# Kernel tuning notes

Measured on AMD Instinct MI355X. Metric: run time of the kernel, lower is better.

The kernel has to match this reference:

```python
import jax, jax.numpy as jnp
import numpy as np

N, E = 100000, 1600000
IN, H, OUT, EA = 128, 128, 128, 128
NUM_LAYERS = 4
EPS = 1e-5


def setup_inputs() -> dict:
    key = jax.random.key(0)
    ks = jax.random.split(key, 12)
    s = 0.05  # small init scale for numerical sanity
    inp = {
        "x": jax.random.normal(ks[0], (N, IN), jnp.float32),
        "edge_index": jax.random.randint(ks[1], (2, E), 0, N, dtype=jnp.int32),
        "edge_attr": jax.random.normal(ks[2], (E, EA), jnp.float32),
        # MLP linears: in->H, H->H, H->H, H->OUT
        "W0": jax.random.normal(ks[3], (H, IN), jnp.float32) * s,
        "b0": jnp.zeros((H,), jnp.float32),
        "W1": jax.random.normal(ks[4], (H, H), jnp.float32) * s,
        "b1": jnp.zeros((H,), jnp.float32),
        "W2": jax.random.normal(ks[5], (H, H), jnp.float32) * s,
        "b2": jnp.zeros((H,), jnp.float32),
        "W3": jax.random.normal(ks[6], (OUT, H), jnp.float32) * s,
        "b3": jnp.zeros((OUT,), jnp.float32),
        # EdgeConv linear: concat(x_j[H], edge_attr[EA]) -> H
        "Wc": jax.random.normal(ks[7], (H, H + EA), jnp.float32) * s,
        "bc": jnp.zeros((H,), jnp.float32),
        # BatchNorm (eval mode: running stats)
        "bn_gamma": jnp.ones((H,), jnp.float32),
        "bn_beta": jnp.zeros((H,), jnp.float32),
        "bn_mean": jnp.zeros((H,), jnp.float32),
        "bn_var": jnp.ones((H,), jnp.float32),
    }
    return inp


def _edge_conv(h, src, dst, ea, deg_inv, Wc, bc):
    # message: lin(concat(x_j, edge_attr)) per edge; aggregate: mean over dst
    msg = jnp.concatenate([h[src], ea], axis=1) @ Wc.T + bc  # [E+N, H]
    agg = jax.ops.segment_sum(msg, dst, num_segments=N)      # [N, H]
    return agg * deg_inv[:, None]


def reference(x, edge_index, edge_attr, W0, b0, W1, b1, W2, b2, W3, b3,
              Wc, bc, bn_gamma, bn_beta, bn_mean, bn_var):
    loop = jnp.arange(N, dtype=edge_index.dtype)
    src = jnp.concatenate([edge_index[0], loop])  # self-loops appended
    dst = jnp.concatenate([edge_index[1], loop])
    ea = jnp.concatenate([edge_attr, jnp.zeros((N, EA), edge_attr.dtype)], axis=0)
    deg = jax.ops.segment_sum(jnp.ones((src.shape[0],), x.dtype), dst, num_segments=N)
    deg_inv = 1.0 / deg  # >= 1 thanks to self-loops

    layers = [(W0, b0), (W1, b1), (W2, b2), (W3, b3)]
    h = x
    for i, (W, b) in enumerate(layers):
        h = h @ W.T                                   # [N, H]
        h = _edge_conv(h, src, dst, ea, deg_inv, Wc, bc)  # eval-mode propagation
        h = h + b
        if i != NUM_LAYERS - 1:
            # BatchNorm1d eval: normalize by running stats
            h = (h - bn_mean) * jax.lax.rsqrt(bn_var + EPS) * bn_gamma + bn_beta
            h = jnp.tanh(h)
            # dropout p=0.0 / eval mode: no-op
    return h
```

## Files before the change

### kernel.cpp

```cpp
#include <hip/hip_runtime.h>
#include <hip/hip_bf16.h>
#include <math.h>

#define NN 100000
#define EE 1600000
#define HD 128
#define MAXDEG 64
#define EPS_BN 1e-5f

typedef __attribute__((ext_vector_type(8))) short short8;
typedef __attribute__((ext_vector_type(4))) float f32x4;

__device__ inline float bf_hi(unsigned u) { return __uint_as_float(u & 0xffff0000u); }
__device__ inline float bf_lo(unsigned u) { return __uint_as_float(u << 16); }
__device__ inline unsigned pack_bf2(float x0, float x1) {
    __hip_bfloat16 a = __float2bfloat16(x0);
    __hip_bfloat16 b = __float2bfloat16(x1);
    unsigned short ua = *reinterpret_cast<unsigned short*>(&a);
    unsigned short ub = *reinterpret_cast<unsigned short*>(&b);
    return (unsigned)ua | ((unsigned)ub << 16);
}

__global__ __launch_bounds__(256) void mega_k(const float* __restrict__ x, unsigned* __restrict__ xb,
                                              const int* __restrict__ src, const int* __restrict__ dst,
                                              int* __restrict__ cursor, int2* __restrict__ list,
                                              const float* __restrict__ W0, const float* __restrict__ W1,
                                              const float* __restrict__ W2, const float* __restrict__ W3,
                                              const float* __restrict__ Wc,
                                              __hip_bfloat16* __restrict__ Mb,
                                              __hip_bfloat16* __restrict__ Wceb) {
    int t = blockIdx.x * 256 + threadIdx.x;
    {
        size_t base = (size_t)t * 8;
        float4 a = *(const float4*)&x[base];
        float4 b = *(const float4*)&x[base + 4];
        uint4 w;
        w.x = pack_bf2(a.x, a.y); w.y = pack_bf2(a.z, a.w);
        w.z = pack_bf2(b.x, b.y); w.w = pack_bf2(b.z, b.w);
        *(uint4*)&xb[(size_t)t * 4] = w;
    }
    {
        int v = dst[t];
        int p = atomicAdd(&cursor[v], 1);
        if (p < MAXDEG) list[(size_t)v * MAXDEG + p] = make_int2(t, src[t]);
    }
    if (blockIdx.x < 320) {
        int part = blockIdx.x >> 6;
        int idx = ((blockIdx.x & 63) << 8) + threadIdx.x;
        int o = idx >> 7, k = idx & 127;
        if (part < 4) {
            const float* W = (part == 0) ? W0 : (part == 1) ? W1 : (part == 2) ? W2 : W3;
            float s = 0.f;
            for (int j = 0; j < 128; ++j) s += Wc[o * 256 + j] * W[j * 128 + k];
            Mb[part * 16384 + idx] = __float2bfloat16(s);
        } else {
            Wceb[idx] = __float2bfloat16(Wc[o * 256 + 128 + k]);
        }
    }
}

__global__ __launch_bounds__(256) void agg_ea_k(const float* __restrict__ ea,
                                                const int* __restrict__ deg, const int2* __restrict__ list,
                                                unsigned* __restrict__ A) {
    int v = blockIdx.x * 4 + (threadIdx.x >> 6);
    int lane = threadIdx.x & 63;
    int grp = lane >> 5, lr = lane & 31;
    if (v >= NN) return;
    size_t o = (size_t)v * MAXDEG;
    int d = deg[v]; if (d > MAXDEG) d = MAXDEG;
    float a0 = 0.f, a1 = 0.f, a2 = 0.f, a3 = 0.f;
    float c0 = 0.f, c1 = 0.f, c2 = 0.f, c3 = 0.f;
    int j = grp;
    for (; j + 6 < d; j += 8) {
        int e0 = list[o + j].x;
        int e1 = list[o + j + 2].x;
        int e2 = list[o + j + 4].x;
        int e3 = list[o + j + 6].x;
        float4 r0 = *(const float4*)&ea[(size_t)e0 * HD + lr * 4];
        float4 r1 = *(const float4*)&ea[(size_t)e1 * HD + lr * 4];
        float4 r2 = *(const float4*)&ea[(size_t)e2 * HD + lr * 4];
        float4 r3 = *(const float4*)&ea[(size_t)e3 * HD + lr * 4];
        a0 += r0.x + r1.x; a1 += r0.y + r1.y; a2 += r0.z + r1.z; a3 += r0.w + r1.w;
        c0 += r2.x + r3.x; c1 += r2.y + r3.y; c2 += r2.z + r3.z; c3 += r2.w + r3.w;
    }
    for (; j + 2 < d; j += 4) {
        int e0 = list[o + j].x;
        int e1 = list[o + j + 2].x;
        float4 r0 = *(const float4*)&ea[(size_t)e0 * HD + lr * 4];
        float4 r1 = *(const float4*)&ea[(size_t)e1 * HD + lr * 4];
        a0 += r0.x + r1.x; a1 += r0.y + r1.y; a2 += r0.z + r1.z; a3 += r0.w + r1.w;
    }
    for (; j < d; j += 2) {
        int e = list[o + j].x;
        float4 r = *(const float4*)&ea[(size_t)e * HD + lr * 4];
        a0 += r.x; a1 += r.y; a2 += r.z; a3 += r.w;
    }
    a0 += c0; a1 += c1; a2 += c2; a3 += c3;
    a0 += __shfl_xor(a0, 32); a1 += __shfl_xor(a1, 32);
    a2 += __shfl_xor(a2, 32); a3 += __shfl_xor(a3, 32);
    if (grp == 0) {
        uint2 w;
        w.x = pack_bf2(a0, a1); w.y = pack_bf2(a2, a3);
        *(uint2*)&A[(size_t)v * 64 + lr * 2] = w;
    }
}

__global__ __launch_bounds__(256) void gather_sum_k(const unsigned* __restrict__ tab,
                                                    const int* __restrict__ deg, const int2* __restrict__ list,
                                                    unsigned* __restrict__ S) {
    int v = blockIdx.x * 4 + (threadIdx.x >> 6);
    int lane = threadIdx.x & 63;
    int grp = lane >> 4, lr = lane & 15;
    if (v >= NN) return;
    size_t o = (size_t)v * MAXDEG;
    int d = deg[v]; if (d > MAXDEG) d = MAXDEG;
    float acc[8], acc2[8];
    {
        uint4 r = *(const uint4*)&tab[(size_t)v * 64 + lr * 4];
        bool m = (grp == 0);
        acc[0] = m ? bf_lo(r.x) : 0.f; acc[1] = m ? bf_hi(r.x) : 0.f;
        acc[2] = m ? bf_lo(r.y) : 0.f; acc[3] = m ? bf_hi(r.y) : 0.f;
        acc[4] = m ? bf_lo(r.z) : 0.f; acc[5] = m ? bf_hi(r.z) : 0.f;
        acc[6] = m ? bf_lo(r.w) : 0.f; acc[7] = m ? bf_hi(r.w) : 0.f;
    }
#pragma unroll
    for (int i = 0; i < 8; ++i) acc2[i] = 0.f;
    int j = grp;
    for (; j + 12 < d; j += 16) {
        int s0 = list[o + j].y;
        int s1 = list[o + j + 4].y;
        int s2 = list[o + j + 8].y;
        int s3 = list[o + j + 12].y;
        uint4 r0 = *(const uint4*)&tab[(size_t)s0 * 64 + lr * 4];
        uint4 r1 = *(const uint4*)&tab[(size_t)s1 * 64 + lr * 4];
        uint4 r2 = *(const uint4*)&tab[(size_t)s2 * 64 + lr * 4];
        uint4 r3 = *(const uint4*)&tab[(size_t)s3 * 64 + lr * 4];
        acc[0] += bf_lo(r0.x) + bf_lo(r1.x); acc[1] += bf_hi(r0.x) + bf_hi(r1.x);
        acc[2] += bf_lo(r0.y) + bf_lo(r1.y); acc[3] += bf_hi(r0.y) + bf_hi(r1.y);
        acc[4] += bf_lo(r0.z) + bf_lo(r1.z); acc[5] += bf_hi(r0.z) + bf_hi(r1.z);
        acc[6] += bf_lo(r0.w) + bf_lo(r1.w); acc[7] += bf_hi(r0.w) + bf_hi(r1.w);
        acc2[0] += bf_lo(r2.x) + bf_lo(r3.x); acc2[1] += bf_hi(r2.x) + bf_hi(r3.x);
        acc2[2] += bf_lo(r2.y) + bf_lo(r3.y); acc2[3] += bf_hi(r2.y) + bf_hi(r3.y);
        acc2[4] += bf_lo(r2.z) + bf_lo(r3.z); acc2[5] += bf_hi(r2.z) + bf_hi(r3.z);
        acc2[6] += bf_lo(r2.w) + bf_lo(r3.w); acc2[7] += bf_hi(r2.w) + bf_hi(r3.w);
    }
    for (; j + 4 < d; j += 8) {
        int s0 = list[o + j].y;
        int s1 = list[o + j + 4].y;
        uint4 r0 = *(const uint4*)&tab[(size_t)s0 * 64 + lr * 4];
        uint4 r1 = *(const uint4*)&tab[(size_t)s1 * 64 + lr * 4];
        acc[0] += bf_lo(r0.x) + bf_lo(r1.x); acc[1] += bf_hi(r0.x) + bf_hi(r1.x);
        acc[2] += bf_lo(r0.y) + bf_lo(r1.y); acc[3] += bf_hi(r0.y) + bf_hi(r1.y);
        acc[4] += bf_lo(r0.z) + bf_lo(r1.z); acc[5] += bf_hi(r0.z) + bf_hi(r1.z);
        acc[6] += bf_lo(r0.w) + bf_lo(r1.w); acc[7] += bf_hi(r0.w) + bf_hi(r1.w);
    }
    for (; j < d; j += 4) {
        int s = list[o + j].y;
        uint4 r = *(const uint4*)&tab[(size_t)s * 64 + lr * 4];
        acc[0] += bf_lo(r.x); acc[1] += bf_hi(r.x);
        acc[2] += bf_lo(r.y); acc[3] += bf_hi(r.y);
        acc[4] += bf_lo(r.z); acc[5] += bf_hi(r.z);
        acc[6] += bf_lo(r.w); acc[7] += bf_hi(r.w);
    }
#pragma unroll
    for (int i = 0; i < 8; ++i) {
        acc[i] += acc2[i];
        acc[i] += __shfl_xor(acc[i], 16);
        acc[i] += __shfl_xor(acc[i], 32);
    }
    if (grp == 0) {
        uint4 w;
        w.x = pack_bf2(acc[0], acc[1]); w.y = pack_bf2(acc[2], acc[3]);
        w.z = pack_bf2(acc[4], acc[5]); w.w = pack_bf2(acc[6], acc[7]);
        *(uint4*)&S[(size_t)v * 64 + lr * 4] = w;
    }
}

template <int MODE>
__global__ __launch_bounds__(256) void gemm_epi_k(const __hip_bfloat16* __restrict__ Sb,
                                                  const __hip_bfloat16* __restrict__ Bw,
                                                  uint2* __restrict__ Usw,
                                                  const int* __restrict__ deg,
                                                  const float* __restrict__ bias,
                                                  const float* __restrict__ bng, const float* __restrict__ bnb,
                                                  const float* __restrict__ bnm, const float* __restrict__ bnv,
                                                  void* __restrict__ out) {
    int wave = threadIdx.x >> 6, lane = threadIdx.x & 63;
    int r0 = blockIdx.x * 64 + wave * 16;
    int R = blockIdx.x * 4 + wave;
    int lr = lane & 15, lg = lane >> 4;

    f32x4 acc[8];
#pragma unroll
    for (int i = 0; i < 8; ++i) acc[i] = (f32x4){0.f, 0.f, 0.f, 0.f};

    int arow = r0 + lr;
    if (arow >= NN) arow = NN - 1;

#pragma unroll
    for (int kb = 0; kb < 4; ++kb) {
        int kofs = kb * 32 + lg * 8;
        short8 a = *(const short8*)(Sb + (size_t)arow * HD + kofs);
#pragma unroll
        for (int fr = 0; fr < 8; ++fr) {
            short8 b = *(const short8*)(Bw + (size_t)(fr * 16 + lr) * HD + kofs);
            acc[fr] = __builtin_amdgcn_mfma_f32_16x16x32_bf16(a, b, acc[fr], 0, 0, 0);
        }
    }

    float di[4];
#pragma unroll
    for (int j = 0; j < 4; ++j) {
        int grow = r0 + lg * 4 + j;
        int d = deg[(grow < NN) ? grow : (NN - 1)];
        di[j] = 1.0f / (float)(d + 1);
    }
#pragma unroll
    for (int fr = 0; fr < 8; ++fr) {
        int col = fr * 16 + lr;
        float bs = bias[col];
        if (MODE == 0) {
            float v0 = acc[fr][0] * di[0] + bs;
            float v1 = acc[fr][1] * di[1] + bs;
            float v2 = acc[fr][2] * di[2] + bs;
            float v3 = acc[fr][3] * di[3] + bs;
            uint2 w;
            w.x = pack_bf2(v0, v1); w.y = pack_bf2(v2, v3);
            Usw[((R * 8 + fr) * 4 + lg) * 16 + lr] = w;
        } else {
            uint2 uu = Usw[((R * 8 + fr) * 4 + lg) * 16 + lr];
            float uv[4] = {bf_lo(uu.x), bf_hi(uu.x), bf_lo(uu.y), bf_hi(uu.y)};
            float me = 0.f, sc = 0.f, be = 0.f;
            if (MODE == 1) {
                me = bnm[col];
                sc = bng[col] * rsqrtf(bnv[col] + EPS_BN);
                be = bnb[col];
            }
#pragma unroll
            for (int j = 0; j < 4; ++j) {
                int grow = r0 + lg * 4 + j;
                if (grow >= NN) continue;
                float val = acc[fr][j] * di[j] + bs + uv[j];
                if (MODE == 1) {
                    val = tanhf((val - me) * sc + be);
                    ((__hip_bfloat16*)out)[(size_t)grow * HD + col] = __float2bfloat16(val);
                } else {
                    ((float*)out)[(size_t)grow * HD + col] = val;
                }
            }
        }
    }
}

extern "C" void kernel_launch(void* const* d_in, const int* in_sizes, int n_in,
                              void* d_out, int out_size, void* d_ws, size_t ws_size,
                              hipStream_t stream) {
    const float* x   = (const float*)d_in[0];
    const int*   ei  = (const int*)d_in[1];
    const float* ea  = (const float*)d_in[2];
    const float* W0  = (const float*)d_in[3];
    const float* b0  = (const float*)d_in[4];
    const float* W1  = (const float*)d_in[5];
    const float* b1  = (const float*)d_in[6];
    const float* W2  = (const float*)d_in[7];
    const float* b2  = (const float*)d_in[8];
    const float* W3  = (const float*)d_in[9];
    const float* b3  = (const float*)d_in[10];
    const float* Wc  = (const float*)d_in[11];
    const float* bc  = (const float*)d_in[12];
    const float* bng = (const float*)d_in[13];
    const float* bnb = (const float*)d_in[14];
    const float* bnm = (const float*)d_in[15];
    const float* bnv = (const float*)d_in[16];

    const int* ei0 = ei;
    const int* ei1 = ei + EE;

    char* ws = (char*)d_ws;
    int*   cursor  = (int*)(ws + 0);
    __hip_bfloat16* Mb   = (__hip_bfloat16*)(ws + 400128);
    __hip_bfloat16* Wceb = (__hip_bfloat16*)(ws + 531200);
    int2*  list    = (int2*)(ws + 564224);
    unsigned* A_b  = (unsigned*)(ws + 51764224);
    uint2* U_sw    = (uint2*)(ws + 77364224);
    unsigned* S_b  = (unsigned*)(ws + 102991872);
    unsigned* h_b  = (unsigned*)(ws + 128591872);
    unsigned* x_b  = (unsigned*)(ws + 154191872);
    (void)ws_size; (void)in_sizes; (void)n_in; (void)out_size;

    hipMemsetAsync(cursor, 0, 400000, stream);

    mega_k<<<EE / 256, 256, 0, stream>>>(x, x_b, ei0, ei1, cursor, list,
                                         W0, W1, W2, W3, Wc, Mb, Wceb);

    agg_ea_k<<<NN / 4, 256, 0, stream>>>(ea, cursor, list, A_b);

    int gblocks = (NN + 63) / 64;
    gemm_epi_k<0><<<gblocks, 256, 0, stream>>>((const __hip_bfloat16*)A_b, Wceb, U_sw,
                                               cursor, bc, nullptr, nullptr, nullptr, nullptr,
                                               nullptr);

    const float* biases[4] = {b0, b1, b2, b3};
    for (int layer = 0; layer < 4; ++layer) {
        const unsigned* tab = (layer == 0) ? x_b : h_b;
        gather_sum_k<<<NN / 4, 256, 0, stream>>>(tab, cursor, list, S_b);
        if (layer < 3) {
            gemm_epi_k<1><<<gblocks, 256, 0, stream>>>((const __hip_bfloat16*)S_b, Mb + layer * 16384,
                                                       U_sw, cursor, biases[layer],
                                                       bng, bnb, bnm, bnv, (void*)h_b);
        } else {
            gemm_epi_k<2><<<gblocks, 256, 0, stream>>>((const __hip_bfloat16*)S_b, Mb + layer * 16384,
                                                       U_sw, cursor, biases[layer],
                                                       nullptr, nullptr, nullptr, nullptr, d_out);
        }
    }
}
```

Before: 742.5 us.

## Split node range and co-schedule gather with GEMM in mixed kernels

Merges the gather-sum and GEMM-epilogue kernels into a single mixed kernel whose blocks do either GEMM rows or neighbour gathers. Nodes are split into two halves. The GEMM over the first half runs alongside the gather for the second half, and layer 0's gather runs alongside the edge-attribute GEMM. The hidden-state buffer is ping-ponged so a layer's output never overwrites the table still being gathered from. This hides the memory-bound gather behind the compute-bound GEMM, at the cost of more launches and heterogeneous blocks that may balance poorly.

```diff
diff --git a/kernel.cpp b/kernel.cpp
--- a/kernel.cpp
+++ b/kernel.cpp
@@ -6,6 +6,7 @@
 #define EE 1600000
 #define HD 128
 #define MAXDEG 64
+#define HB 50048
 #define EPS_BN 1e-5f
 
 typedef __attribute__((ext_vector_type(8))) short short8;
@@ -105,26 +106,22 @@
     }
 }
 
-__global__ __launch_bounds__(256) void gather_sum_k(const unsigned* __restrict__ tab,
-                                                    const int* __restrict__ deg, const int2* __restrict__ list,
-                                                    unsigned* __restrict__ S) {
-    int v = blockIdx.x * 4 + (threadIdx.x >> 6);
-    int lane = threadIdx.x & 63;
+__device__ __forceinline__ void gather_body(const unsigned* __restrict__ tab, const int* __restrict__ deg,
+                                            const int2* __restrict__ list, unsigned* __restrict__ S,
+                                            int v, int lane) {
     int grp = lane >> 4, lr = lane & 15;
-    if (v >= NN) return;
     size_t o = (size_t)v * MAXDEG;
     int d = deg[v]; if (d > MAXDEG) d = MAXDEG;
     float acc[8], acc2[8];
-    {
+#pragma unroll
+    for (int i = 0; i < 8; ++i) { acc[i] = 0.f; acc2[i] = 0.f; }
+    if (grp == 0) {
         uint4 r = *(const uint4*)&tab[(size_t)v * 64 + lr * 4];
-        bool m = (grp == 0);
-        acc[0] = m ? bf_lo(r.x) : 0.f; acc[1] = m ? bf_hi(r.x) : 0.f;
-        acc[2] = m ? bf_lo(r.y) : 0.f; acc[3] = m ? bf_hi(r.y) : 0.f;
-        acc[4] = m ? bf_lo(r.z) : 0.f; acc[5] = m ? bf_hi(r.z) : 0.f;
-        acc[6] = m ? bf_lo(r.w) : 0.f; acc[7] = m ? bf_hi(r.w) : 0.f;
-    }
-#pragma unroll
-    for (int i = 0; i < 8; ++i) acc2[i] = 0.f;
+        acc[0] = bf_lo(r.x); acc[1] = bf_hi(r.x);
+        acc[2] = bf_lo(r.y); acc[3] = bf_hi(r.y);
+        acc[4] = bf_lo(r.z); acc[5] = bf_hi(r.z);
+        acc[6] = bf_lo(r.w); acc[7] = bf_hi(r.w);
+    }
     int j = grp;
     for (; j + 12 < d; j += 16) {
         int s0 = list[o + j].y;
@@ -177,17 +174,18 @@
 }
 
 template <int MODE>
-__global__ __launch_bounds__(256) void gemm_epi_k(const __hip_bfloat16* __restrict__ Sb,
-                                                  const __hip_bfloat16* __restrict__ Bw,
-                                                  uint2* __restrict__ Usw,
-                                                  const int* __restrict__ deg,
-                                                  const float* __restrict__ bias,
-                                                  const float* __restrict__ bng, const float* __restrict__ bnb,
-                                                  const float* __restrict__ bnm, const float* __restrict__ bnv,
-                                                  void* __restrict__ out) {
+__device__ __forceinline__ void gemm_body(int bLocal, int rowBase,
+                                          const __hip_bfloat16* __restrict__ Sb,
+                                          const __hip_bfloat16* __restrict__ Bw,
+                                          uint2* __restrict__ Usw,
+                                          const int* __restrict__ deg,
+                                          const float* __restrict__ bias,
+                                          const float* __restrict__ bng, const float* __restrict__ bnb,
+                                          const float* __restrict__ bnm, const float* __restrict__ bnv,
+                                          void* __restrict__ out) {
     int wave = threadIdx.x >> 6, lane = threadIdx.x & 63;
-    int r0 = blockIdx.x * 64 + wave * 16;
-    int R = blockIdx.x * 4 + wave;
+    int r0 = rowBase + bLocal * 64 + wave * 16;
+    int R = r0 >> 4;
     int lr = lane & 15, lg = lane >> 4;
 
     f32x4 acc[8];
@@ -252,6 +250,27 @@
     }
 }
 
+template <int MODE>
+__global__ __launch_bounds__(256) void mixed_k(int ngemm, int rowBase,
+                                               const __hip_bfloat16* __restrict__ Sb,
+                                               const __hip_bfloat16* __restrict__ Bw,
+                                               uint2* __restrict__ Usw,
+                                               const int* __restrict__ deg,
+                                               const float* __restrict__ bias,
+                                               const float* __restrict__ bng, const float* __restrict__ bnb,
+                                               const float* __restrict__ bnm, const float* __restrict__ bnv,
+                                               void* __restrict__ out,
+                                               const unsigned* __restrict__ tab, int nodeBase,
+                                               unsigned* __restrict__ Sout,
+                                               const int2* __restrict__ list) {
+    if ((int)blockIdx.x < ngemm) {
+        gemm_body<MODE>(blockIdx.x, rowBase, Sb, Bw, Usw, deg, bias, bng, bnb, bnm, bnv, out);
+    } else {
+        int v = nodeBase + (blockIdx.x - ngemm) * 4 + (threadIdx.x >> 6);
+        if (v < NN) gather_body(tab, deg, list, Sout, v, threadIdx.x & 63);
+    }
+}
+
 extern "C" void kernel_launch(void* const* d_in, const int* in_sizes, int n_in,
                               void* d_out, int out_size, void* d_ws, size_t ws_size,
                               hipStream_t stream) {
@@ -284,9 +303,16 @@
     unsigned* A_b  = (unsigned*)(ws + 51764224);
     uint2* U_sw    = (uint2*)(ws + 77364224);
     unsigned* S_b  = (unsigned*)(ws + 102991872);
-    unsigned* h_b  = (unsigned*)(ws + 128591872);
-    unsigned* x_b  = (unsigned*)(ws + 154191872);
+    unsigned* hA   = (unsigned*)(ws + 128591872);
+    unsigned* hB   = (unsigned*)(ws + 154191872);
+    unsigned* x_b  = (unsigned*)(ws + 179791872);
     (void)ws_size; (void)in_sizes; (void)n_in; (void)out_size;
+
+    const int G1N = HB / 64;
+    const int G2N = (NN - HB + 63) / 64;
+    const int GA1 = HB / 4;
+    const int GA2 = (NN - HB + 3) / 4;
+    const int GFULL = (NN + 63) / 64;
 
     hipMemsetAsync(cursor, 0, 400000, stream);
 
@@ -295,23 +321,41 @@
 
     agg_ea_k<<<NN / 4, 256, 0, stream>>>(ea, cursor, list, A_b);
 
-    int gblocks = (NN + 63) / 64;
-    gemm_epi_k<0><<<gblocks, 256, 0, stream>>>((const __hip_bfloat16*)A_b, Wceb, U_sw,
-                                               cursor, bc, nullptr, nullptr, nullptr, nullptr,
-                                               nullptr);
+    mixed_k<0><<<GFULL + GA1, 256, 0, stream>>>(GFULL, 0,
+        (const __hip_bfloat16*)A_b, Wceb, U_sw, cursor, bc,
+        nullptr, nullptr, nullptr, nullptr, nullptr,
+        x_b, 0, S_b, list);
 
     const float* biases[4] = {b0, b1, b2, b3};
+    const unsigned* tabs[4] = {x_b, hA, hB, hA};
+    unsigned* outs[3] = {hA, hB, hA};
+
     for (int layer = 0; layer < 4; ++layer) {
-        const unsigned* tab = (layer == 0) ? x_b : h_b;
-        gather_sum_k<<<NN / 4, 256, 0, stream>>>(tab, cursor, list, S_b);
+        const unsigned* tab = tabs[layer];
+        if (layer > 0) {
+            mixed_k<1><<<GA1, 256, 0, stream>>>(0, 0,
+                nullptr, nullptr, U_sw, cursor, biases[layer],
+                nullptr, nullptr, nullptr, nullptr, nullptr,
+                tab, 0, S_b, list);
+        }
         if (layer < 3) {
-            gemm_epi_k<1><<<gblocks, 256, 0, stream>>>((const __hip_bfloat16*)S_b, Mb + layer * 16384,
-                                                       U_sw, cursor, biases[layer],
-                                                       bng, bnb, bnm, bnv, (void*)h_b);
+            mixed_k<1><<<G1N + GA2, 256, 0, stream>>>(G1N, 0,
+                (const __hip_bfloat16*)S_b, Mb + layer * 16384, U_sw, cursor, biases[layer],
+                bng, bnb, bnm, bnv, (void*)outs[layer],
+                tab, HB, S_b, list);
+            mixed_k<1><<<G2N, 256, 0, stream>>>(G2N, HB,
+                (const __hip_bfloat16*)S_b, Mb + layer * 16384, U_sw, cursor, biases[layer],
+                bng, bnb, bnm, bnv, (void*)outs[layer],
+                tab, HB, S_b, list);
         } else {
-            gemm_epi_k<2><<<gblocks, 256, 0, stream>>>((const __hip_bfloat16*)S_b, Mb + layer * 16384,
-                                                       U_sw, cursor, biases[layer],
-                                                       nullptr, nullptr, nullptr, nullptr, d_out);
-        }
-    }
-}
+            mixed_k<2><<<G1N + GA2, 256, 0, stream>>>(G1N, 0,
+                (const __hip_bfloat16*)S_b, Mb + layer * 16384, U_sw, cursor, biases[layer],
+                nullptr, nullptr, nullptr, nullptr, d_out,
+                tab, HB, S_b, list);
+            mixed_k<2><<<G2N, 256, 0, stream>>>(G2N, HB,
+                (const __hip_bfloat16*)S_b, Mb + layer * 16384, U_sw, cursor, biases[layer],
+                nullptr, nullptr, nullptr, nullptr, d_out,
+                tab, HB, S_b, list);
+        }
+    }
+}
```

Measured after the change: 841.6 us. 13.3% more time.
